# Optimization experiments

Measured on AMD Instinct MI355X. Metric: run time of the kernel, lower is better.

## Reference

```python
import jax, jax.numpy as jnp
import numpy as np


def setup_inputs() -> dict:
    key = jax.random.key(0)
    k1, k2 = jax.random.split(key)
    N, P1, P2, D = 4, 8192, 8192, 3
    source_cloud = jax.random.normal(k1, (N, P1, D), dtype=jnp.float32)
    target_cloud = jax.random.normal(k2, (N, P2, D), dtype=jnp.float32)
    return {"source_cloud": source_cloud, "target_cloud": target_cloud}


def reference(source_cloud, target_cloud):
    # ChamferDistance.forward with defaults:
    #   bidirectional=False, reverse=False -> single-directional x->y
    #   point_reduction='sum', batch_reduction='mean', norm=2, no normals/weights
    x, y = source_cloud, target_cloud  # (N,P1,D), (N,P2,D)
    x2 = jnp.sum(x * x, axis=-1)                       # (N,P1)
    y2 = jnp.sum(y * y, axis=-1)                       # (N,P2)
    xy = jnp.einsum('npd,nqd->npq', x, y)              # (N,P1,P2)
    d2 = x2[:, :, None] + y2[None if False else slice(None), None, :] - 2.0 * xy  # (N,P1,P2)
    # squared L2 distances are non-negative; clamp tiny negatives from the GEMM trick
    nn_d2 = jnp.maximum(jnp.min(d2, axis=-1), 0.0)     # (N,P1) 1-NN squared dist
    per_cloud = jnp.sum(nn_d2, axis=1)                 # point_reduction='sum'
    loss = jnp.mean(per_cloud)                         # batch_reduction='mean'
    return loss
```

## Files before the change

### kernel.cpp

```cpp
#include <hip/hip_runtime.h>
#include <float.h>

typedef float float2v __attribute__((ext_vector_type(2)));
typedef float float4v __attribute__((ext_vector_type(4)));

#define N_BATCH 4
#define P1 8192
#define P2 8192
#define D 3

#define CHUNK 128
#define NCHUNK (P2 / CHUNK)
#define NSTEP (CHUNK / 4)
#define RSRC 8
#define TPB 256
#define SRC_PER_BLK (TPB * RSRC)
#define NSRCBLK (P1 / SRC_PER_BLK)
#define NMIN (N_BATCH * P1)

#define TPB_R 128

__global__ __launch_bounds__(TPB, 4) void chamfer_main(
        const float* __restrict__ src,
        const float* __restrict__ tgt,
        float* __restrict__ ws,
        float* __restrict__ out) {
    const int bid = blockIdx.x;
    const int c   = bid % NCHUNK;
    const int sb  = (bid / NCHUNK) % NSRCBLK;
    const int n   = bid / (NCHUNK * NSRCBLK);
    const int t   = threadIdx.x;

    if (bid == 0 && t == 0) out[0] = 0.0f;

    __shared__ __align__(16) float sT[4 * CHUNK];

    if (t < CHUNK) {
        const int j = c * CHUNK + t;
        const float* p = tgt + ((size_t)n * P2 + j) * D;
        const float y0 = p[0], y1 = p[1], y2 = p[2];
        sT[t]             = -2.0f * y0;
        sT[CHUNK + t]     = -2.0f * y1;
        sT[2 * CHUNK + t] = -2.0f * y2;
        sT[3 * CHUNK + t] = y0 * y0 + y1 * y1 + y2 * y2;
    }
    __syncthreads();

    float2v bx0[RSRC], bx1[RSRC], bx2[RSRC];
    float m[RSRC];
#pragma unroll
    for (int i = 0; i < RSRC; ++i) {
        const int s = sb * SRC_PER_BLK + i * TPB + t;
        const float* p = src + ((size_t)n * P1 + s) * D;
        bx0[i] = (float2v){p[0], p[0]};
        bx1[i] = (float2v){p[1], p[1]};
        bx2[i] = (float2v){p[2], p[2]};
        m[i] = FLT_MAX;
    }

    const int w = t >> 6;
    const int start = ((w << 3) | (((bid >> 8) & 3) << 1)) & (NSTEP - 1);

#pragma unroll 4
    for (int s = 0; s < NSTEP; ++s) {
        const int step = (s + start) & (NSTEP - 1);
        const int fb = step * 4;
        const float4v X = *(const float4v*)&sT[fb];
        const float4v Y = *(const float4v*)&sT[CHUNK + fb];
        const float4v Z = *(const float4v*)&sT[2 * CHUNK + fb];
        const float4v W = *(const float4v*)&sT[3 * CHUNK + fb];
#pragma unroll
        for (int i = 0; i < RSRC; ++i) {
            float2v d;
            d = __builtin_elementwise_fma(bx0[i], X.xy, W.xy);
            d = __builtin_elementwise_fma(bx1[i], Y.xy, d);
            d = __builtin_elementwise_fma(bx2[i], Z.xy, d);
            m[i] = fminf(fminf(m[i], d.x), d.y);
            d = __builtin_elementwise_fma(bx0[i], X.zw, W.zw);
            d = __builtin_elementwise_fma(bx1[i], Y.zw, d);
            d = __builtin_elementwise_fma(bx2[i], Z.zw, d);
            m[i] = fminf(fminf(m[i], d.x), d.y);
        }
    }

#pragma unroll
    for (int i = 0; i < RSRC; ++i) {
        const int s = n * P1 + sb * SRC_PER_BLK + i * TPB + t;
        ws[(size_t)c * NMIN + s] = m[i];
    }
}

__global__ __launch_bounds__(TPB_R) void chamfer_reduce(
        const float* __restrict__ ws,
        const float* __restrict__ src,
        float* __restrict__ out) {
    const int gid = blockIdx.x * TPB_R + threadIdx.x;

    float v[NCHUNK];
#pragma unroll
    for (int c = 0; c < NCHUNK; ++c)
        v[c] = ws[(size_t)c * NMIN + gid];
#pragma unroll
    for (int s = NCHUNK / 2; s > 0; s >>= 1)
#pragma unroll
        for (int c = 0; c < s; ++c)
            v[c] = fminf(v[c], v[c + s]);

    const float* p = src + (size_t)gid * D;
    const float xs = p[0] * p[0] + p[1] * p[1] + p[2] * p[2];
    float r = fmaxf(v[0] + xs, 0.0f);

#pragma unroll
    for (int off = 32; off > 0; off >>= 1)
        r += __shfl_down(r, off, 64);
    __shared__ float sred[TPB_R / 64];
    const int lane = threadIdx.x & 63;
    const int w    = threadIdx.x >> 6;
    if (lane == 0) sred[w] = r;
    __syncthreads();
    if (threadIdx.x == 0) {
        float s = 0.0f;
#pragma unroll
        for (int i = 0; i < TPB_R / 64; ++i) s += sred[i];
        atomicAdd(out, s * (1.0f / N_BATCH));
    }
}

extern "C" void kernel_launch(void* const* d_in, const int* in_sizes, int n_in,
                              void* d_out, int out_size, void* d_ws, size_t ws_size,
                              hipStream_t stream) {
    const float* src = (const float*)d_in[0];
    const float* tgt = (const float*)d_in[1];
    float* out = (float*)d_out;
    float* ws  = (float*)d_ws;

    const int nblocks = N_BATCH * NSRCBLK * NCHUNK;
    chamfer_main<<<nblocks, TPB, 0, stream>>>(src, tgt, ws, out);

    chamfer_reduce<<<NMIN / TPB_R, TPB_R, 0, stream>>>(ws, src, out);
}
```

Baseline: 35.73 us.

## Halve per-thread source rows, raise occupancy, and split the chunk reduction across lanes

The main kernel now keeps 4 source points per thread instead of 8 and allows 8 blocks per CU, which doubles the block count. Block indexing is flattened across batches with shifts and masks, and the staggered LDS start offset is removed. The reduce kernel now gives each point 8 lanes: each lane takes the min over 8 chunk partials and a width-8 xor shuffle combines them, which adds more parallelism than one thread walking 64 partials. In exchange, each LDS load feeds fewer FMAs, and the reduce reads from the workspace are less coalesced.

Measured after the change: 45.34 us. 1.27x slower.

```diff
diff --git a/kernel.cpp b/kernel.cpp
--- a/kernel.cpp
+++ b/kernel.cpp
@@ -11,24 +11,21 @@
 
 #define CHUNK 128
 #define NCHUNK (P2 / CHUNK)
-#define NSTEP (CHUNK / 4)
-#define RSRC 8
+#define RSRC 4
 #define TPB 256
 #define SRC_PER_BLK (TPB * RSRC)
-#define NSRCBLK (P1 / SRC_PER_BLK)
+#define NSB (N_BATCH * P1 / SRC_PER_BLK)
 #define NMIN (N_BATCH * P1)
 
-#define TPB_R 128
-
-__global__ __launch_bounds__(TPB, 4) void chamfer_main(
+__global__ __launch_bounds__(TPB, 8) void chamfer_main(
         const float* __restrict__ src,
         const float* __restrict__ tgt,
         float* __restrict__ ws,
         float* __restrict__ out) {
     const int bid = blockIdx.x;
-    const int c   = bid % NCHUNK;
-    const int sb  = (bid / NCHUNK) % NSRCBLK;
-    const int n   = bid / (NCHUNK * NSRCBLK);
+    const int c   = bid & (NCHUNK - 1);
+    const int sb  = bid >> 6;
+    const int n   = sb >> 3;
     const int t   = threadIdx.x;
 
     if (bid == 0 && t == 0) out[0] = 0.0f;
@@ -51,19 +48,15 @@
 #pragma unroll
     for (int i = 0; i < RSRC; ++i) {
         const int s = sb * SRC_PER_BLK + i * TPB + t;
-        const float* p = src + ((size_t)n * P1 + s) * D;
+        const float* p = src + (size_t)s * D;
         bx0[i] = (float2v){p[0], p[0]};
         bx1[i] = (float2v){p[1], p[1]};
         bx2[i] = (float2v){p[2], p[2]};
         m[i] = FLT_MAX;
     }
 
-    const int w = t >> 6;
-    const int start = ((w << 3) | (((bid >> 8) & 3) << 1)) & (NSTEP - 1);
-
 #pragma unroll 4
-    for (int s = 0; s < NSTEP; ++s) {
-        const int step = (s + start) & (NSTEP - 1);
+    for (int step = 0; step < CHUNK / 4; ++step) {
         const int fb = step * 4;
         const float4v X = *(const float4v*)&sT[fb];
         const float4v Y = *(const float4v*)&sT[CHUNK + fb];
@@ -85,44 +78,48 @@
 
 #pragma unroll
     for (int i = 0; i < RSRC; ++i) {
-        const int s = n * P1 + sb * SRC_PER_BLK + i * TPB + t;
+        const int s = sb * SRC_PER_BLK + i * TPB + t;
         ws[(size_t)c * NMIN + s] = m[i];
     }
 }
 
-__global__ __launch_bounds__(TPB_R) void chamfer_reduce(
+__global__ __launch_bounds__(TPB) void chamfer_reduce(
         const float* __restrict__ ws,
         const float* __restrict__ src,
         float* __restrict__ out) {
-    const int gid = blockIdx.x * TPB_R + threadIdx.x;
+    const int gid = blockIdx.x * TPB + threadIdx.x;
+    const int s = gid >> 3;
+    const int k = gid & 7;
 
-    float v[NCHUNK];
+    float m = ws[(size_t)(k * 8) * NMIN + s];
 #pragma unroll
-    for (int c = 0; c < NCHUNK; ++c)
-        v[c] = ws[(size_t)c * NMIN + gid];
+    for (int j = 1; j < 8; ++j)
+        m = fminf(m, ws[(size_t)(k * 8 + j) * NMIN + s]);
+
 #pragma unroll
-    for (int s = NCHUNK / 2; s > 0; s >>= 1)
-#pragma unroll
-        for (int c = 0; c < s; ++c)
-            v[c] = fminf(v[c], v[c + s]);
+    for (int off = 4; off > 0; off >>= 1)
+        m = fminf(m, __shfl_xor(m, off, 8));
 
-    const float* p = src + (size_t)gid * D;
-    const float xs = p[0] * p[0] + p[1] * p[1] + p[2] * p[2];
-    float r = fmaxf(v[0] + xs, 0.0f);
+    float r = 0.0f;
+    if (k == 0) {
+        const float* p = src + (size_t)s * D;
+        const float xs = p[0] * p[0] + p[1] * p[1] + p[2] * p[2];
+        r = fmaxf(m + xs, 0.0f);
+    }
 
 #pragma unroll
     for (int off = 32; off > 0; off >>= 1)
         r += __shfl_down(r, off, 64);
-    __shared__ float sred[TPB_R / 64];
+    __shared__ float sred[TPB / 64];
     const int lane = threadIdx.x & 63;
     const int w    = threadIdx.x >> 6;
     if (lane == 0) sred[w] = r;
     __syncthreads();
     if (threadIdx.x == 0) {
-        float s = 0.0f;
+        float acc = 0.0f;
 #pragma unroll
-        for (int i = 0; i < TPB_R / 64; ++i) s += sred[i];
-        atomicAdd(out, s * (1.0f / N_BATCH));
+        for (int i = 0; i < TPB / 64; ++i) acc += sred[i];
+        atomicAdd(out, acc * (1.0f / N_BATCH));
     }
 }
 
@@ -134,8 +131,8 @@
     float* out = (float*)d_out;
     float* ws  = (float*)d_ws;
 
-    const int nblocks = N_BATCH * NSRCBLK * NCHUNK;
+    const int nblocks = NSB * NCHUNK;
     chamfer_main<<<nblocks, TPB, 0, stream>>>(src, tgt, ws, out);
 
-    chamfer_reduce<<<NMIN / TPB_R, TPB_R, 0, stream>>>(ws, src, out);
+    chamfer_reduce<<<NMIN * 8 / TPB, TPB, 0, stream>>>(ws, src, out);
 }
```

## Halve target chunk size, drop LDS start staggering, stream reduce over chunks

Applied to the files above, without the earlier changes.

Halves the target chunk per block from 128 to 64, which doubles the block count and the number of partial-min planes written to the workspace. It raises the launch-bounds occupancy hint, and it removes the per-wave staggered start offset into shared memory. Source coordinates are now kept as scalars and splatted inline, and block indices are decoded with shifts. The reduce kernel folds a running min over the chunks instead of holding an array tree, and uses 256 threads per block. The cost is twice the workspace traffic and possible LDS bank conflicts now that the staggering is gone.

Result: slower. 109.2 us (+205.7%).

```diff
diff --git a/kernel.cpp b/kernel.cpp
--- a/kernel.cpp
+++ b/kernel.cpp
@@ -9,26 +9,26 @@
 #define P2 8192
 #define D 3
 
-#define CHUNK 128
+#define CHUNK 64
 #define NCHUNK (P2 / CHUNK)
 #define NSTEP (CHUNK / 4)
 #define RSRC 8
 #define TPB 256
 #define SRC_PER_BLK (TPB * RSRC)
-#define NSRCBLK (P1 / SRC_PER_BLK)
+#define NSB (N_BATCH * P1 / SRC_PER_BLK)
 #define NMIN (N_BATCH * P1)
 
-#define TPB_R 128
+#define TPB_R 256
 
-__global__ __launch_bounds__(TPB, 4) void chamfer_main(
+__global__ __launch_bounds__(TPB, 6) void chamfer_main(
         const float* __restrict__ src,
         const float* __restrict__ tgt,
         float* __restrict__ ws,
         float* __restrict__ out) {
     const int bid = blockIdx.x;
-    const int c   = bid % NCHUNK;
-    const int sb  = (bid / NCHUNK) % NSRCBLK;
-    const int n   = bid / (NCHUNK * NSRCBLK);
+    const int c   = bid & (NCHUNK - 1);
+    const int sb  = bid >> 7;
+    const int n   = sb >> 2;
     const int t   = threadIdx.x;
 
     if (bid == 0 && t == 0) out[0] = 0.0f;
@@ -46,24 +46,17 @@
     }
     __syncthreads();
 
-    float2v bx0[RSRC], bx1[RSRC], bx2[RSRC];
-    float m[RSRC];
+    float x0[RSRC], x1[RSRC], x2[RSRC], m[RSRC];
 #pragma unroll
     for (int i = 0; i < RSRC; ++i) {
         const int s = sb * SRC_PER_BLK + i * TPB + t;
-        const float* p = src + ((size_t)n * P1 + s) * D;
-        bx0[i] = (float2v){p[0], p[0]};
-        bx1[i] = (float2v){p[1], p[1]};
-        bx2[i] = (float2v){p[2], p[2]};
+        const float* p = src + (size_t)s * D;
+        x0[i] = p[0]; x1[i] = p[1]; x2[i] = p[2];
         m[i] = FLT_MAX;
     }
 
-    const int w = t >> 6;
-    const int start = ((w << 3) | (((bid >> 8) & 3) << 1)) & (NSTEP - 1);
-
-#pragma unroll 4
-    for (int s = 0; s < NSTEP; ++s) {
-        const int step = (s + start) & (NSTEP - 1);
+#pragma unroll 2
+    for (int step = 0; step < NSTEP; ++step) {
         const int fb = step * 4;
         const float4v X = *(const float4v*)&sT[fb];
         const float4v Y = *(const float4v*)&sT[CHUNK + fb];
@@ -72,20 +65,20 @@
 #pragma unroll
         for (int i = 0; i < RSRC; ++i) {
             float2v d;
-            d = __builtin_elementwise_fma(bx0[i], X.xy, W.xy);
-            d = __builtin_elementwise_fma(bx1[i], Y.xy, d);
-            d = __builtin_elementwise_fma(bx2[i], Z.xy, d);
+            d = __builtin_elementwise_fma((float2v){x0[i], x0[i]}, X.xy, W.xy);
+            d = __builtin_elementwise_fma((float2v){x1[i], x1[i]}, Y.xy, d);
+            d = __builtin_elementwise_fma((float2v){x2[i], x2[i]}, Z.xy, d);
             m[i] = fminf(fminf(m[i], d.x), d.y);
-            d = __builtin_elementwise_fma(bx0[i], X.zw, W.zw);
-            d = __builtin_elementwise_fma(bx1[i], Y.zw, d);
-            d = __builtin_elementwise_fma(bx2[i], Z.zw, d);
+            d = __builtin_elementwise_fma((float2v){x0[i], x0[i]}, X.zw, W.zw);
+            d = __builtin_elementwise_fma((float2v){x1[i], x1[i]}, Y.zw, d);
+            d = __builtin_elementwise_fma((float2v){x2[i], x2[i]}, Z.zw, d);
             m[i] = fminf(fminf(m[i], d.x), d.y);
         }
     }
 
 #pragma unroll
     for (int i = 0; i < RSRC; ++i) {
-        const int s = n * P1 + sb * SRC_PER_BLK + i * TPB + t;
+        const int s = sb * SRC_PER_BLK + i * TPB + t;
         ws[(size_t)c * NMIN + s] = m[i];
     }
 }
@@ -96,19 +89,14 @@
         float* __restrict__ out) {
     const int gid = blockIdx.x * TPB_R + threadIdx.x;
 
-    float v[NCHUNK];
-#pragma unroll
+    float m = FLT_MAX;
+#pragma unroll 8
     for (int c = 0; c < NCHUNK; ++c)
-        v[c] = ws[(size_t)c * NMIN + gid];
-#pragma unroll
-    for (int s = NCHUNK / 2; s > 0; s >>= 1)
-#pragma unroll
-        for (int c = 0; c < s; ++c)
-            v[c] = fminf(v[c], v[c + s]);
+        m = fminf(m, ws[(size_t)c * NMIN + gid]);
 
     const float* p = src + (size_t)gid * D;
     const float xs = p[0] * p[0] + p[1] * p[1] + p[2] * p[2];
-    float r = fmaxf(v[0] + xs, 0.0f);
+    float r = fmaxf(m + xs, 0.0f);
 
 #pragma unroll
     for (int off = 32; off > 0; off >>= 1)
@@ -134,7 +122,7 @@
     float* out = (float*)d_out;
     float* ws  = (float*)d_ws;
 
-    const int nblocks = N_BATCH * NSRCBLK * NCHUNK;
+    const int nblocks = NSB * NCHUNK;
     chamfer_main<<<nblocks, TPB, 0, stream>>>(src, tgt, ws, out);
 
     chamfer_reduce<<<NMIN / TPB_R, TPB_R, 0, stream>>>(ws, src, out);
```
